# Kernel tuning notes

Hardware: AMD Instinct MI355X
Metric: run time of the kernel (lower is better)

The kernel has to match this reference:

```python
import jax, jax.numpy as jnp
import numpy as np

B, N, C, H = 4, 2048, 1024, 16
D = C // H  # head_dim = 64

def setup_inputs() -> dict:
    key = jax.random.key(0)
    k1, k2, k3, k4, k5, k6 = jax.random.split(key, 6)
    x = jax.random.normal(k1, (B, N, C), dtype=jnp.float32)
    rope_cos = jax.random.uniform(k2, (N, D), dtype=jnp.float32)
    rope_sin = jax.random.uniform(k3, (N, D), dtype=jnp.float32)
    w_qkv = jax.random.normal(k4, (3 * C, C), dtype=jnp.float32) * (C ** -0.5)
    w_proj = jax.random.normal(k5, (C, C), dtype=jnp.float32) * (C ** -0.5)
    b_proj = jax.random.normal(k6, (C,), dtype=jnp.float32) * 0.01
    return {"x": x, "rope_cos": rope_cos, "rope_sin": rope_sin,
            "w_qkv": w_qkv, "w_proj": w_proj, "b_proj": b_proj}

def _rotate_half(x):
    x1, x2 = jnp.split(x, 2, axis=-1)
    return jnp.concatenate((-x2, x1), axis=-1)

def _apply_rope(x, cos, sin):
    # x: [B,H,N,D]; cos/sin: [N,D] broadcast over B,H
    return x * cos + _rotate_half(x) * sin

def reference(x, rope_cos, rope_sin, w_qkv, w_proj, b_proj):
    Bc, Nc, Cc = x.shape
    scale = D ** -0.5
    qkv = jnp.einsum('bnc,fc->bnf', x, w_qkv)            # [B,N,3C]
    qkv = qkv.reshape(Bc, Nc, 3, H, D).transpose(2, 0, 3, 1, 4)  # [3,B,H,N,D]
    q, k, v = qkv[0], qkv[1], qkv[2]
    q = _apply_rope(q, rope_cos, rope_sin)
    k = _apply_rope(k, rope_cos, rope_sin)
    attn = jnp.einsum('bhnd,bhmd->bhnm', q, k) * scale   # [B,H,N,N]
    attn = jax.nn.softmax(attn, axis=-1)
    out = jnp.einsum('bhnm,bhmd->bhnd', attn, v)         # [B,H,N,D]
    out = out.transpose(0, 2, 1, 3).reshape(Bc, Nc, Cc)  # [B,N,C]
    return jnp.einsum('bnc,fc->bnf', out, w_proj) + b_proj
```

## Files before the change

### kernel.cpp

```cpp
#include <hip/hip_runtime.h>

#define MM   8192
#define CC   1024
#define F3   3072
#define NN   2048
#define HH   16
#define DD   64
#define QSCALE 0.1803368801111731f

typedef __attribute__((ext_vector_type(8))) __bf16 bf16x8;
typedef __attribute__((ext_vector_type(4))) float floatx4;
typedef __attribute__((ext_vector_type(4))) unsigned uintx4;

__device__ __forceinline__ unsigned short f2b(float f) {
  union { float f; unsigned int u; } v; v.f = f;
  unsigned int r = v.u + 0x7fffu + ((v.u >> 16) & 1u);
  return (unsigned short)(r >> 16);
}
__device__ __forceinline__ float b2f(unsigned short b) {
  union { unsigned int u; float f; } v; v.u = ((unsigned int)b) << 16;
  return v.f;
}

__device__ __forceinline__ void gl_lds16(const unsigned short* g, unsigned short* l) {
  __builtin_amdgcn_global_load_lds((const __attribute__((address_space(1))) void*)g,
                                   (__attribute__((address_space(3))) void*)l, 16, 0, 0);
}

__global__ __launch_bounds__(256) void f32_to_bf16_k(const float* __restrict__ in,
                                                     unsigned short* __restrict__ out, int n4) {
  int i = blockIdx.x * 256 + threadIdx.x;
  if (i < n4) {
    float4 v = ((const float4*)in)[i];
    ushort4 o;
    o.x = f2b(v.x); o.y = f2b(v.y); o.z = f2b(v.z); o.w = f2b(v.w);
    ((ushort4*)out)[i] = o;
  }
}

template <int F, bool BF16OUT, bool ROPE>
__global__ __launch_bounds__(512, 2) void gemm_p(const unsigned short* __restrict__ A,
                                                 const unsigned short* __restrict__ Bm,
                                                 void* __restrict__ Cout,
                                                 const float* __restrict__ bias,
                                                 const float* __restrict__ rcp,
                                                 const float* __restrict__ spp, int K) {
  __shared__ alignas(16) unsigned short lA[3][128 * 64];
  __shared__ alignas(16) unsigned short lB[3][256 * 64];
  const int tid = threadIdx.x, lane = tid & 63, wave = tid >> 6;
  const int r16 = lane & 15, q4 = lane >> 4;
  const int wm = wave & 1, wn = wave >> 1;

  const int id = blockIdx.x;
  const int xcd = id & 7, slot = id >> 3;
  const int rx = xcd * 8 + (slot & 7), cy = slot >> 3;
  const int rowBase = rx * 128, colBase = cy * 256;

  const int cA0 = tid, cA1 = tid + 512;
  const int cB0 = tid, cB1 = tid + 512, cB2 = tid + 1024, cB3 = tid + 1536;
#define CHOFF(base, c) ((size_t)((base) + ((c) >> 3)) * K + ((((c) & 7) ^ (((c) >> 3) & 7)) << 3))
  const size_t aoff0 = CHOFF(rowBase, cA0), aoff1 = CHOFF(rowBase, cA1);
  const size_t boff0 = CHOFF(colBase, cB0), boff1 = CHOFF(colBase, cB1);
  const size_t boff2 = CHOFF(colBase, cB2), boff3 = CHOFF(colBase, cB3);
#undef CHOFF

#define STAGEP(kt, bsel) do { const int _k0 = (kt) * 64; \
    gl_lds16(A + aoff0 + _k0, &lA[bsel][cA0 * 8]); \
    gl_lds16(A + aoff1 + _k0, &lA[bsel][cA1 * 8]); \
    gl_lds16(Bm + boff0 + _k0, &lB[bsel][cB0 * 8]); \
    gl_lds16(Bm + boff1 + _k0, &lB[bsel][cB1 * 8]); \
    gl_lds16(Bm + boff2 + _k0, &lB[bsel][cB2 * 8]); \
    gl_lds16(Bm + boff3 + _k0, &lB[bsel][cB3 * 8]); } while (0)

  floatx4 acc[4][4];
  const floatx4 z = {0.f, 0.f, 0.f, 0.f};
#pragma unroll
  for (int i = 0; i < 4; ++i)
#pragma unroll
    for (int j = 0; j < 4; ++j) acc[i][j] = z;

  const int nt = K / 64;

  STAGEP(0, 0);
  STAGEP(1, 1);
  STAGEP(2, 2);
  asm volatile("s_waitcnt vmcnt(12)" ::: "memory");
  __builtin_amdgcn_s_barrier();
  __builtin_amdgcn_sched_barrier(0);

  int bs = 0;
  for (int t = 0; t < nt; ++t) {
    const unsigned short* la = &lA[bs][0];
    const unsigned short* lb = &lB[bs][0];
    bf16x8 af[4][2], bv[4][2];
#pragma unroll
    for (int im = 0; im < 4; ++im) {
      int row = wm * 64 + im * 16 + r16, r7 = row & 7;
      af[im][0] = *(const bf16x8*)(la + row * 64 + ((q4 ^ r7) << 3));
      af[im][1] = *(const bf16x8*)(la + row * 64 + (((4 + q4) ^ r7) << 3));
    }
#pragma unroll
    for (int jf = 0; jf < 4; ++jf) {
      int row = wn * 64 + jf * 16 + r16, r7 = row & 7;
      bv[jf][0] = *(const bf16x8*)(lb + row * 64 + ((q4 ^ r7) << 3));
      bv[jf][1] = *(const bf16x8*)(lb + row * 64 + (((4 + q4) ^ r7) << 3));
    }
    __builtin_amdgcn_s_setprio(1);
#pragma unroll
    for (int jf = 0; jf < 4; ++jf)
#pragma unroll
      for (int im = 0; im < 4; ++im) {
        acc[im][jf] = __builtin_amdgcn_mfma_f32_16x16x32_bf16(af[im][0], bv[jf][0], acc[im][jf], 0, 0, 0);
        acc[im][jf] = __builtin_amdgcn_mfma_f32_16x16x32_bf16(af[im][1], bv[jf][1], acc[im][jf], 0, 0, 0);
      }
    __builtin_amdgcn_s_setprio(0);

    __builtin_amdgcn_s_barrier();
    __builtin_amdgcn_sched_barrier(0);
    if (t + 3 < nt) {
      STAGEP(t + 3, bs);
      asm volatile("s_waitcnt vmcnt(12)" ::: "memory");
    } else {
      asm volatile("s_waitcnt vmcnt(0)" ::: "memory");
    }
    __builtin_amdgcn_sched_barrier(0);
    __builtin_amdgcn_s_barrier();
    __builtin_amdgcn_sched_barrier(0);
    bs = (bs == 2) ? 0 : bs + 1;
  }
#undef STAGEP

  if (ROPE) {
    int head = (colBase >> 6) + wn;
    if (head < 32) {
      const bool isq = head < 16;
#pragma unroll
      for (int im = 0; im < 4; ++im)
#pragma unroll
        for (int jf = 0; jf < 2; ++jf)
#pragma unroll
          for (int r = 0; r < 4; ++r) {
            int grow = rowBase + wm * 64 + im * 16 + q4 * 4 + r;
            int n = grow & (NN - 1);
            int dp = jf * 16 + r16;
            float x0 = acc[im][jf][r], x1 = acc[im][jf + 2][r];
            float c0 = rcp[n * DD + dp],      s0v = spp[n * DD + dp];
            float c1 = rcp[n * DD + dp + 32], s1v = spp[n * DD + dp + 32];
            float y0 = x0 * c0 - x1 * s0v;
            float y1 = x1 * c1 + x0 * s1v;
            if (isq) { y0 *= QSCALE; y1 *= QSCALE; }
            acc[im][jf][r] = y0;
            acc[im][jf + 2][r] = y1;
          }
    }
  }

#pragma unroll
  for (int im = 0; im < 4; ++im)
#pragma unroll
    for (int jf = 0; jf < 4; ++jf)
#pragma unroll
      for (int r = 0; r < 4; ++r) {
        int grow = rowBase + wm * 64 + im * 16 + q4 * 4 + r;
        int gcol = colBase + wn * 64 + jf * 16 + r16;
        if (BF16OUT)
          ((unsigned short*)Cout)[(size_t)grow * F + gcol] = f2b(acc[im][jf][r]);
        else
          ((float*)Cout)[(size_t)grow * F + gcol] = acc[im][jf][r] + bias[gcol];
      }
}

__global__ __launch_bounds__(256, 4) void attn_k(const unsigned short* __restrict__ qkv,
                                                 unsigned short* __restrict__ obuf) {
  __shared__ alignas(16) unsigned short sK[64 * 64];
  __shared__ alignas(16) unsigned short sVT[64 * 64];

  const int tid = threadIdx.x, lane = tid & 63, wave = tid >> 6;
  const int r16 = lane & 15, q4 = lane >> 4;

  const int id = blockIdx.x + (int)gridDim.x * blockIdx.y;
  const int xcd = id & 7, slot = id >> 3;
  const int bh = xcd * 8 + (slot >> 4);
  const int q0 = (slot & 15) * 128;
  const int b = bh >> 4, h = bh & 15;
  const unsigned short* qbase = qkv + (size_t)(b * NN) * F3 + h * DD;

  bf16x8 qf[2][2];
#pragma unroll
  for (int im = 0; im < 2; ++im)
#pragma unroll
    for (int kk = 0; kk < 2; ++kk)
      qf[im][kk] = *(const bf16x8*)(qbase +
          (size_t)(q0 + wave * 32 + im * 16 + r16) * F3 + kk * 32 + q4 * 8);

  const floatx4 z = {0.f, 0.f, 0.f, 0.f};
  floatx4 o[2][4];
  float lacc[2] = {0.f, 0.f};
#pragma unroll
  for (int im = 0; im < 2; ++im)
    for (int jd = 0; jd < 4; ++jd) o[im][jd] = z;

  const int krow0 = tid >> 3, kc8 = tid & 7;
  const int vkvp = tid >> 3, vc8 = tid & 7;
  const int mp = (vkvp & 16) | ((vkvp & 4) << 1) | ((vkvp & 2) << 1) |
                 ((vkvp & 8) >> 2) | (vkvp & 1);

  const unsigned short* kvb = qbase;
  int4 kreg0 = *(const int4*)(kvb + (size_t)krow0 * F3 + CC + kc8 * 8);
  int4 kreg1 = *(const int4*)(kvb + (size_t)(krow0 + 32) * F3 + CC + kc8 * 8);
  int4 vreg0 = *(const int4*)(kvb + (size_t)(2 * vkvp) * F3 + 2 * CC + vc8 * 8);
  int4 vreg1 = *(const int4*)(kvb + (size_t)(2 * vkvp + 1) * F3 + 2 * CC + vc8 * 8);

  for (int t = 0; t < NN / 64; ++t) {
    __syncthreads();

    *(int4*)(&sK[krow0 * 64 + ((kc8 ^ (krow0 & 7)) << 3)]) = kreg0;
    *(int4*)(&sK[(krow0 + 32) * 64 + ((kc8 ^ ((krow0 + 32) & 7)) << 3)]) = kreg1;
    {
      const unsigned* a0 = (const unsigned*)&vreg0;
      const unsigned* a1 = (const unsigned*)&vreg1;
#pragma unroll
      for (int w = 0; w < 4; ++w) {
        unsigned lo = __builtin_amdgcn_perm(a1[w], a0[w], 0x05040100u);
        unsigned hi = __builtin_amdgcn_perm(a1[w], a0[w], 0x07060302u);
        int d0 = vc8 * 8 + 2 * w;
        int sw0 = (2 * w + vc8) & 7;
        int sw1 = (2 * w + 1 + vc8) & 7;
        *(unsigned*)(&sVT[d0 * 64 + (((mp >> 2) ^ sw0) << 3) + 2 * (mp & 3)]) = lo;
        *(unsigned*)(&sVT[(d0 + 1) * 64 + (((mp >> 2) ^ sw1) << 3) + 2 * (mp & 3)]) = hi;
      }
    }

    if (t + 1 < NN / 64) {
      const unsigned short* nb = qkv + (size_t)(b * NN + (t + 1) * 64) * F3 + h * DD;
      kreg0 = *(const int4*)(nb + (size_t)krow0 * F3 + CC + kc8 * 8);
      kreg1 = *(const int4*)(nb + (size_t)(krow0 + 32) * F3 + CC + kc8 * 8);
      vreg0 = *(const int4*)(nb + (size_t)(2 * vkvp) * F3 + 2 * CC + vc8 * 8);
      vreg1 = *(const int4*)(nb + (size_t)(2 * vkvp + 1) * F3 + 2 * CC + vc8 * 8);
    }

    __syncthreads();

    floatx4 s[2][4];
    __builtin_amdgcn_s_setprio(1);
#pragma unroll
    for (int jn = 0; jn < 4; ++jn) {
      int row = jn * 16 + r16;
      bf16x8 kf0 = *(const bf16x8*)(&sK[row * 64 + ((q4 ^ (row & 7)) << 3)]);
      bf16x8 kf1 = *(const bf16x8*)(&sK[row * 64 + (((4 + q4) ^ (row & 7)) << 3)]);
#pragma unroll
      for (int im = 0; im < 2; ++im) {
        floatx4 a = z;
        a = __builtin_amdgcn_mfma_f32_16x16x32_bf16(kf0, qf[im][0], a, 0, 0, 0);
        a = __builtin_amdgcn_mfma_f32_16x16x32_bf16(kf1, qf[im][1], a, 0, 0, 0);
        s[im][jn] = a;
      }
    }
    __builtin_amdgcn_s_setprio(0);

    bf16x8 pf[2][2];
#pragma unroll
    for (int im = 0; im < 2; ++im) {
#pragma unroll
      for (int kk = 0; kk < 2; ++kk) {
        uintx4 pk;
#pragma unroll
        for (int j2 = 0; j2 < 2; ++j2) {
          int jn = 2 * kk + j2;
          float p0 = __builtin_amdgcn_exp2f(s[im][jn][0]);
          float p1 = __builtin_amdgcn_exp2f(s[im][jn][1]);
          float p2 = __builtin_amdgcn_exp2f(s[im][jn][2]);
          float p3 = __builtin_amdgcn_exp2f(s[im][jn][3]);
          lacc[im] += (p0 + p1) + (p2 + p3);
          asm("v_cvt_pk_bf16_f32 %0, %1, %2" : "=v"(pk[2 * j2]) : "v"(p0), "v"(p1));
          asm("v_cvt_pk_bf16_f32 %0, %1, %2" : "=v"(pk[2 * j2 + 1]) : "v"(p2), "v"(p3));
        }
        pf[im][kk] = __builtin_bit_cast(bf16x8, pk);
      }
    }

    __builtin_amdgcn_s_setprio(1);
#pragma unroll
    for (int jd = 0; jd < 4; ++jd) {
      int d = jd * 16 + r16;
      int swr = (d + (d >> 3)) & 7;
      bf16x8 vf0 = *(const bf16x8*)(&sVT[d * 64 + ((q4 ^ swr) << 3)]);
      bf16x8 vf1 = *(const bf16x8*)(&sVT[d * 64 + (((4 + q4) ^ swr) << 3)]);
#pragma unroll
      for (int im = 0; im < 2; ++im) {
        o[im][jd] = __builtin_amdgcn_mfma_f32_16x16x32_bf16(pf[im][0], vf0, o[im][jd], 0, 0, 0);
        o[im][jd] = __builtin_amdgcn_mfma_f32_16x16x32_bf16(pf[im][1], vf1, o[im][jd], 0, 0, 0);
      }
    }
    __builtin_amdgcn_s_setprio(0);
  }

#pragma unroll
  for (int im = 0; im < 2; ++im) {
    float l = lacc[im];
    l += __shfl_xor(l, 16);
    l += __shfl_xor(l, 32);
    float inv = 1.0f / l;
#pragma unroll
    for (int r = 0; r < 4; ++r) {
      float invr = __shfl(inv, q4 * 4 + r);
      int row = q0 + wave * 32 + im * 16 + q4 * 4 + r;
#pragma unroll
      for (int jd = 0; jd < 4; ++jd) {
        int col = h * DD + jd * 16 + r16;
        obuf[(size_t)(b * NN + row) * CC + col] = f2b(o[im][jd][r] * invr);
      }
    }
  }
}

extern "C" void kernel_launch(void* const* d_in, const int* in_sizes, int n_in,
                              void* d_out, int out_size, void* d_ws, size_t ws_size,
                              hipStream_t stream) {
  const float* x     = (const float*)d_in[0];
  const float* rc    = (const float*)d_in[1];
  const float* rs    = (const float*)d_in[2];
  const float* wqkv  = (const float*)d_in[3];
  const float* wproj = (const float*)d_in[4];
  const float* bproj = (const float*)d_in[5];
  float* out = (float*)d_out;

  char* w = (char*)d_ws;
  unsigned short* xb     = (unsigned short*)(w);
  unsigned short* wqkvb  = (unsigned short*)(w + 16777216);
  unsigned short* wprojb = (unsigned short*)(w + 23068672);
  unsigned short* qkvb   = (unsigned short*)(w + 25165824);
  unsigned short* obuf   = (unsigned short*)(w + 75497472);

  f32_to_bf16_k<<<(MM * CC / 4 + 255) / 256, 256, 0, stream>>>(x, xb, MM * CC / 4);
  f32_to_bf16_k<<<(F3 * CC / 4 + 255) / 256, 256, 0, stream>>>(wqkv, wqkvb, F3 * CC / 4);
  f32_to_bf16_k<<<(CC * CC / 4 + 255) / 256, 256, 0, stream>>>(wproj, wprojb, CC * CC / 4);

  gemm_p<F3, true, true><<<768, 512, 0, stream>>>(
      xb, wqkvb, qkvb, nullptr, rc, rs, CC);

  attn_k<<<dim3(NN / 128, 4 * HH), 256, 0, stream>>>(qkvb, obuf);

  gemm_p<CC, false, false><<<256, 512, 0, stream>>>(
      obuf, wprojb, out, bproj, nullptr, nullptr, CC);
}
```

Before: 279.2 us.

## Use 256x256 tile double-buffered GEMM for QKV projection with fused RoPE

```diff
diff --git a/kernel.cpp b/kernel.cpp
--- a/kernel.cpp
+++ b/kernel.cpp
@@ -36,6 +36,137 @@
     o.x = f2b(v.x); o.y = f2b(v.y); o.z = f2b(v.z); o.w = f2b(v.w);
     ((ushort4*)out)[i] = o;
   }
+}
+
+template <int F, bool BF16OUT, bool ROPE>
+__global__ __launch_bounds__(512, 2) void gemm256(const unsigned short* __restrict__ A,
+                                                  const unsigned short* __restrict__ Bm,
+                                                  void* __restrict__ Cout,
+                                                  const float* __restrict__ bias,
+                                                  const float* __restrict__ rcp,
+                                                  const float* __restrict__ spp, int K) {
+  __shared__ alignas(16) unsigned short lA[2][256 * 64];
+  __shared__ alignas(16) unsigned short lB[2][256 * 64];
+  const int tid = threadIdx.x, lane = tid & 63, wave = tid >> 6;
+  const int r16 = lane & 15, q4 = lane >> 4;
+  const int wm = wave & 1, wn = wave >> 1;
+
+  const int id = blockIdx.x;
+  const int xcd = id & 7, slot = id >> 3;
+  const int rx = xcd * 4 + (slot & 3), cy = slot >> 2;
+  const int rowBase = rx * 256, colBase = cy * 256;
+
+#define CHOFF(base, c) ((size_t)((base) + ((c) >> 3)) * K + ((((c) & 7) ^ (((c) >> 3) & 7)) << 3))
+  size_t aoff[4], boff[4];
+#pragma unroll
+  for (int i = 0; i < 4; ++i) {
+    aoff[i] = CHOFF(rowBase, tid + i * 512);
+    boff[i] = CHOFF(colBase, tid + i * 512);
+  }
+#undef CHOFF
+
+#define STAGEP(kt, bsel) do { const int _k0 = (kt) * 64; \
+    gl_lds16(A + aoff[0] + _k0, &lA[bsel][(tid) * 8]); \
+    gl_lds16(A + aoff[1] + _k0, &lA[bsel][(tid + 512) * 8]); \
+    gl_lds16(A + aoff[2] + _k0, &lA[bsel][(tid + 1024) * 8]); \
+    gl_lds16(A + aoff[3] + _k0, &lA[bsel][(tid + 1536) * 8]); \
+    gl_lds16(Bm + boff[0] + _k0, &lB[bsel][(tid) * 8]); \
+    gl_lds16(Bm + boff[1] + _k0, &lB[bsel][(tid + 512) * 8]); \
+    gl_lds16(Bm + boff[2] + _k0, &lB[bsel][(tid + 1024) * 8]); \
+    gl_lds16(Bm + boff[3] + _k0, &lB[bsel][(tid + 1536) * 8]); } while (0)
+
+  floatx4 acc[8][4];
+  const floatx4 z = {0.f, 0.f, 0.f, 0.f};
+#pragma unroll
+  for (int i = 0; i < 8; ++i)
+#pragma unroll
+    for (int j = 0; j < 4; ++j) acc[i][j] = z;
+
+  const int nt = K / 64;
+
+  STAGEP(0, 0);
+  STAGEP(1, 1);
+  asm volatile("s_waitcnt vmcnt(8)" ::: "memory");
+  __builtin_amdgcn_s_barrier();
+  __builtin_amdgcn_sched_barrier(0);
+
+  for (int t = 0; t < nt; ++t) {
+    const int bs = t & 1;
+    const unsigned short* la = &lA[bs][0];
+    const unsigned short* lb = &lB[bs][0];
+    bf16x8 af[8][2];
+#pragma unroll
+    for (int im = 0; im < 8; ++im) {
+      int row = wm * 128 + im * 16 + r16, r7 = row & 7;
+      af[im][0] = *(const bf16x8*)(la + row * 64 + ((q4 ^ r7) << 3));
+      af[im][1] = *(const bf16x8*)(la + row * 64 + (((4 + q4) ^ r7) << 3));
+    }
+#pragma unroll
+    for (int jf = 0; jf < 4; ++jf) {
+      int row = wn * 64 + jf * 16 + r16, r7 = row & 7;
+      bf16x8 bv0 = *(const bf16x8*)(lb + row * 64 + ((q4 ^ r7) << 3));
+      bf16x8 bv1 = *(const bf16x8*)(lb + row * 64 + (((4 + q4) ^ r7) << 3));
+      __builtin_amdgcn_s_setprio(1);
+#pragma unroll
+      for (int im = 0; im < 8; ++im) {
+        acc[im][jf] = __builtin_amdgcn_mfma_f32_16x16x32_bf16(af[im][0], bv0, acc[im][jf], 0, 0, 0);
+        acc[im][jf] = __builtin_amdgcn_mfma_f32_16x16x32_bf16(af[im][1], bv1, acc[im][jf], 0, 0, 0);
+      }
+      __builtin_amdgcn_s_setprio(0);
+    }
+
+    __builtin_amdgcn_s_barrier();
+    __builtin_amdgcn_sched_barrier(0);
+    if (t + 2 < nt) {
+      STAGEP(t + 2, bs);
+      asm volatile("s_waitcnt vmcnt(8)" ::: "memory");
+    } else {
+      asm volatile("s_waitcnt vmcnt(0)" ::: "memory");
+    }
+    __builtin_amdgcn_sched_barrier(0);
+    __builtin_amdgcn_s_barrier();
+    __builtin_amdgcn_sched_barrier(0);
+  }
+#undef STAGEP
+
+  if (ROPE) {
+    int head = (colBase >> 6) + wn;
+    if (head < 32) {
+      const bool isq = head < 16;
+#pragma unroll
+      for (int im = 0; im < 8; ++im)
+#pragma unroll
+        for (int jf = 0; jf < 2; ++jf)
+#pragma unroll
+          for (int r = 0; r < 4; ++r) {
+            int grow = rowBase + wm * 128 + im * 16 + q4 * 4 + r;
+            int n = grow & (NN - 1);
+            int dp = jf * 16 + r16;
+            float x0 = acc[im][jf][r], x1 = acc[im][jf + 2][r];
+            float c0 = rcp[n * DD + dp],      s0v = spp[n * DD + dp];
+            float c1 = rcp[n * DD + dp + 32], s1v = spp[n * DD + dp + 32];
+            float y0 = x0 * c0 - x1 * s0v;
+            float y1 = x1 * c1 + x0 * s1v;
+            if (isq) { y0 *= QSCALE; y1 *= QSCALE; }
+            acc[im][jf][r] = y0;
+            acc[im][jf + 2][r] = y1;
+          }
+    }
+  }
+
+#pragma unroll
+  for (int im = 0; im < 8; ++im)
+#pragma unroll
+    for (int jf = 0; jf < 4; ++jf)
+#pragma unroll
+      for (int r = 0; r < 4; ++r) {
+        int grow = rowBase + wm * 128 + im * 16 + q4 * 4 + r;
+        int gcol = colBase + wn * 64 + jf * 16 + r16;
+        if (BF16OUT)
+          ((unsigned short*)Cout)[(size_t)grow * F + gcol] = f2b(acc[im][jf][r]);
+        else
+          ((float*)Cout)[(size_t)grow * F + gcol] = acc[im][jf][r] + bias[gcol];
+      }
 }
 
 template <int F, bool BF16OUT, bool ROPE>
@@ -336,7 +467,7 @@
   f32_to_bf16_k<<<(F3 * CC / 4 + 255) / 256, 256, 0, stream>>>(wqkv, wqkvb, F3 * CC / 4);
   f32_to_bf16_k<<<(CC * CC / 4 + 255) / 256, 256, 0, stream>>>(wproj, wprojb, CC * CC / 4);
 
-  gemm_p<F3, true, true><<<768, 512, 0, stream>>>(
+  gemm256<F3, true, true><<<384, 512, 0, stream>>>(
       xb, wqkvb, qkvb, nullptr, rc, rs, CC);
 
   attn_k<<<dim3(NN / 128, 4 * HH), 256, 0, stream>>>(qkvb, obuf);
```

After: 281.7 us. Within noise of the previous version (+0.9%).

## Retile GEMM to 256x128 blocks with 4 waves, K=32, double buffering

Applied to the files above, without the earlier changes.

```diff
diff --git a/kernel.cpp b/kernel.cpp
--- a/kernel.cpp
+++ b/kernel.cpp
@@ -39,94 +39,90 @@
 }
 
 template <int F, bool BF16OUT, bool ROPE>
-__global__ __launch_bounds__(512, 2) void gemm_p(const unsigned short* __restrict__ A,
-                                                 const unsigned short* __restrict__ Bm,
-                                                 void* __restrict__ Cout,
-                                                 const float* __restrict__ bias,
-                                                 const float* __restrict__ rcp,
-                                                 const float* __restrict__ spp, int K) {
-  __shared__ alignas(16) unsigned short lA[3][128 * 64];
-  __shared__ alignas(16) unsigned short lB[3][256 * 64];
+__global__ __launch_bounds__(256, 2) void gemm_v7(const unsigned short* __restrict__ A,
+                                                  const unsigned short* __restrict__ Bm,
+                                                  void* __restrict__ Cout,
+                                                  const float* __restrict__ bias,
+                                                  const float* __restrict__ rcp,
+                                                  const float* __restrict__ spp, int K) {
+  __shared__ alignas(16) unsigned short lA[2][256 * 32];
+  __shared__ alignas(16) unsigned short lB[2][128 * 32];
   const int tid = threadIdx.x, lane = tid & 63, wave = tid >> 6;
   const int r16 = lane & 15, q4 = lane >> 4;
   const int wm = wave & 1, wn = wave >> 1;
 
   const int id = blockIdx.x;
   const int xcd = id & 7, slot = id >> 3;
-  const int rx = xcd * 8 + (slot & 7), cy = slot >> 3;
-  const int rowBase = rx * 128, colBase = cy * 256;
-
-  const int cA0 = tid, cA1 = tid + 512;
-  const int cB0 = tid, cB1 = tid + 512, cB2 = tid + 1024, cB3 = tid + 1536;
-#define CHOFF(base, c) ((size_t)((base) + ((c) >> 3)) * K + ((((c) & 7) ^ (((c) >> 3) & 7)) << 3))
-  const size_t aoff0 = CHOFF(rowBase, cA0), aoff1 = CHOFF(rowBase, cA1);
-  const size_t boff0 = CHOFF(colBase, cB0), boff1 = CHOFF(colBase, cB1);
-  const size_t boff2 = CHOFF(colBase, cB2), boff3 = CHOFF(colBase, cB3);
+  const int rx = xcd * 4 + (slot & 3), cy = slot >> 2;
+  const int rowBase = rx * 256, colBase = cy * 128;
+
+#define CHOFF(base, c) ((size_t)((base) + ((c) >> 2)) * K + (((((c) & 3) ^ (((c) >> 3) & 3))) << 3))
+  size_t aoff[4], boff[2];
+#pragma unroll
+  for (int i = 0; i < 4; ++i) aoff[i] = CHOFF(rowBase, tid + i * 256);
+#pragma unroll
+  for (int i = 0; i < 2; ++i) boff[i] = CHOFF(colBase, tid + i * 256);
 #undef CHOFF
 
-#define STAGEP(kt, bsel) do { const int _k0 = (kt) * 64; \
-    gl_lds16(A + aoff0 + _k0, &lA[bsel][cA0 * 8]); \
-    gl_lds16(A + aoff1 + _k0, &lA[bsel][cA1 * 8]); \
-    gl_lds16(Bm + boff0 + _k0, &lB[bsel][cB0 * 8]); \
-    gl_lds16(Bm + boff1 + _k0, &lB[bsel][cB1 * 8]); \
-    gl_lds16(Bm + boff2 + _k0, &lB[bsel][cB2 * 8]); \
-    gl_lds16(Bm + boff3 + _k0, &lB[bsel][cB3 * 8]); } while (0)
-
-  floatx4 acc[4][4];
+#define STAGEP(kt, bsel) do { const int _k0 = (kt) * 32; \
+    gl_lds16(A + aoff[0] + _k0, &lA[bsel][(tid) * 8]); \
+    gl_lds16(A + aoff[1] + _k0, &lA[bsel][(tid + 256) * 8]); \
+    gl_lds16(A + aoff[2] + _k0, &lA[bsel][(tid + 512) * 8]); \
+    gl_lds16(A + aoff[3] + _k0, &lA[bsel][(tid + 768) * 8]); \
+    gl_lds16(Bm + boff[0] + _k0, &lB[bsel][(tid) * 8]); \
+    gl_lds16(Bm + boff[1] + _k0, &lB[bsel][(tid + 256) * 8]); } while (0)
+
+  floatx4 acc[8][4];
   const floatx4 z = {0.f, 0.f, 0.f, 0.f};
 #pragma unroll
-  for (int i = 0; i < 4; ++i)
+  for (int i = 0; i < 8; ++i)
 #pragma unroll
     for (int j = 0; j < 4; ++j) acc[i][j] = z;
 
-  const int nt = K / 64;
+  const int nt = K / 32;
 
   STAGEP(0, 0);
   STAGEP(1, 1);
-  STAGEP(2, 2);
-  asm volatile("s_waitcnt vmcnt(12)" ::: "memory");
+  asm volatile("s_waitcnt vmcnt(6)" ::: "memory");
   __builtin_amdgcn_s_barrier();
   __builtin_amdgcn_sched_barrier(0);
 
-  int bs = 0;
   for (int t = 0; t < nt; ++t) {
+    const int bs = t & 1;
     const unsigned short* la = &lA[bs][0];
     const unsigned short* lb = &lB[bs][0];
-    bf16x8 af[4][2], bv[4][2];
-#pragma unroll
-    for (int im = 0; im < 4; ++im) {
-      int row = wm * 64 + im * 16 + r16, r7 = row & 7;
-      af[im][0] = *(const bf16x8*)(la + row * 64 + ((q4 ^ r7) << 3));
-      af[im][1] = *(const bf16x8*)(la + row * 64 + (((4 + q4) ^ r7) << 3));
+    bf16x8 af[8], bv[4];
+#pragma unroll
+    for (int im = 0; im < 8; ++im) {
+      int row = wm * 128 + im * 16 + r16;
+      int pc = q4 ^ ((row >> 1) & 3);
+      af[im] = *(const bf16x8*)(la + row * 32 + pc * 8);
     }
 #pragma unroll
     for (int jf = 0; jf < 4; ++jf) {
-      int row = wn * 64 + jf * 16 + r16, r7 = row & 7;
-      bv[jf][0] = *(const bf16x8*)(lb + row * 64 + ((q4 ^ r7) << 3));
-      bv[jf][1] = *(const bf16x8*)(lb + row * 64 + (((4 + q4) ^ r7) << 3));
+      int row = wn * 64 + jf * 16 + r16;
+      int pc = q4 ^ ((row >> 1) & 3);
+      bv[jf] = *(const bf16x8*)(lb + row * 32 + pc * 8);
     }
     __builtin_amdgcn_s_setprio(1);
 #pragma unroll
     for (int jf = 0; jf < 4; ++jf)
 #pragma unroll
-      for (int im = 0; im < 4; ++im) {
-        acc[im][jf] = __builtin_amdgcn_mfma_f32_16x16x32_bf16(af[im][0], bv[jf][0], acc[im][jf], 0, 0, 0);
-        acc[im][jf] = __builtin_amdgcn_mfma_f32_16x16x32_bf16(af[im][1], bv[jf][1], acc[im][jf], 0, 0, 0);
-      }
+      for (int im = 0; im < 8; ++im)
+        acc[im][jf] = __builtin_amdgcn_mfma_f32_16x16x32_bf16(af[im], bv[jf], acc[im][jf], 0, 0, 0);
     __builtin_amdgcn_s_setprio(0);
 
     __builtin_amdgcn_s_barrier();
     __builtin_amdgcn_sched_barrier(0);
-    if (t + 3 < nt) {
-      STAGEP(t + 3, bs);
-      asm volatile("s_waitcnt vmcnt(12)" ::: "memory");
+    if (t + 2 < nt) {
+      STAGEP(t + 2, bs);
+      asm volatile("s_waitcnt vmcnt(6)" ::: "memory");
     } else {
       asm volatile("s_waitcnt vmcnt(0)" ::: "memory");
     }
     __builtin_amdgcn_sched_barrier(0);
     __builtin_amdgcn_s_barrier();
     __builtin_amdgcn_sched_barrier(0);
-    bs = (bs == 2) ? 0 : bs + 1;
   }
 #undef STAGEP
 
@@ -135,12 +131,12 @@
     if (head < 32) {
       const bool isq = head < 16;
 #pragma unroll
-      for (int im = 0; im < 4; ++im)
+      for (int im = 0; im < 8; ++im)
 #pragma unroll
         for (int jf = 0; jf < 2; ++jf)
 #pragma unroll
           for (int r = 0; r < 4; ++r) {
-            int grow = rowBase + wm * 64 + im * 16 + q4 * 4 + r;
+            int grow = rowBase + wm * 128 + im * 16 + q4 * 4 + r;
             int n = grow & (NN - 1);
             int dp = jf * 16 + r16;
             float x0 = acc[im][jf][r], x1 = acc[im][jf + 2][r];
@@ -156,12 +152,12 @@
   }
 
 #pragma unroll
-  for (int im = 0; im < 4; ++im)
+  for (int im = 0; im < 8; ++im)
 #pragma unroll
     for (int jf = 0; jf < 4; ++jf)
 #pragma unroll
       for (int r = 0; r < 4; ++r) {
-        int grow = rowBase + wm * 64 + im * 16 + q4 * 4 + r;
+        int grow = rowBase + wm * 128 + im * 16 + q4 * 4 + r;
         int gcol = colBase + wn * 64 + jf * 16 + r16;
         if (BF16OUT)
           ((unsigned short*)Cout)[(size_t)grow * F + gcol] = f2b(acc[im][jf][r]);
@@ -336,11 +332,11 @@
   f32_to_bf16_k<<<(F3 * CC / 4 + 255) / 256, 256, 0, stream>>>(wqkv, wqkvb, F3 * CC / 4);
   f32_to_bf16_k<<<(CC * CC / 4 + 255) / 256, 256, 0, stream>>>(wproj, wprojb, CC * CC / 4);
 
-  gemm_p<F3, true, true><<<768, 512, 0, stream>>>(
+  gemm_v7<F3, true, true><<<768, 256, 0, stream>>>(
       xb, wqkvb, qkvb, nullptr, rc, rs, CC);
 
   attn_k<<<dim3(NN / 128, 4 * HH), 256, 0, stream>>>(qkvb, obuf);
 
-  gemm_p<CC, false, false><<<256, 512, 0, stream>>>(
+  gemm_v7<CC, false, false><<<256, 256, 0, stream>>>(
       obuf, wprojb, out, bproj, nullptr, nullptr, CC);
 }
```

Result: slower. 294.5 us (+5.5%).
